# Performance work log

Measured on AMD Instinct MI355X. Metric: run time of the kernel, lower is better.

Reference implementation:

```python
import jax, jax.numpy as jnp
import numpy as np
from jax import lax

B, F, H, W = 1, 8, 16, 16
DIM, HEADS, HD, RANK, T = 1920, 30, 64, 128, 226
SV = F * H * W          # 2048 video tokens
S = T + SV              # 2274 total tokens


def setup_inputs() -> dict:
    key = jax.random.key(0)
    ks = jax.random.split(key, 12)
    r = lambda k, sh, s: jax.random.normal(k, sh, dtype=jnp.float32) * s
    theta = jax.random.uniform(ks[0], (SV, HD), dtype=jnp.float32) * (2.0 * np.pi)
    return dict(
        hidden_states=r(ks[1], (B, SV, DIM), 1.0),
        encoder_hidden_states=r(ks[2], (B, T, DIM), 1.0),
        cos=jnp.cos(theta),
        sin=jnp.sin(theta),
        to_q_w=r(ks[3], (DIM, DIM), 0.02), to_q_b=r(ks[4], (DIM,), 0.02),
        to_k_w=r(ks[5], (DIM, DIM), 0.02), to_k_b=r(ks[6], (DIM,), 0.02),
        to_v_w=r(ks[7], (DIM, DIM), 0.02), to_v_b=r(ks[8], (DIM,), 0.02),
        norm_q_w=jnp.ones((HD,), jnp.float32), norm_q_b=jnp.zeros((HD,), jnp.float32),
        norm_k_w=jnp.ones((HD,), jnp.float32), norm_k_b=jnp.zeros((HD,), jnp.float32),
        conv1_w=r(ks[9], (RANK, DIM, 3), 0.05),
        conv2_w=r(ks[10], (DIM, RANK, 3), 0.05),
        to_out_w=r(ks[11], (DIM, DIM), 0.02),
        to_out_b=jnp.zeros((DIM,), jnp.float32),
    )


def _layernorm(x, w, b, eps=1e-6):
    mu = jnp.mean(x, axis=-1, keepdims=True)
    var = jnp.mean(jnp.square(x - mu), axis=-1, keepdims=True)
    return (x - mu) * lax.rsqrt(var + eps) * w + b


def _rope(x, cos, sin):
    # diffusers interleaved RoPE: pairs (even, odd) along last dim
    xr, xi = x[..., 0::2], x[..., 1::2]
    x_rot = jnp.stack([-xi, xr], axis=-1).reshape(x.shape)
    return x * cos + x_rot * sin


def _conv1d(x, w):  # x: [N, C, L], w: [O, I, K], SAME padding
    return lax.conv_general_dilated(x, w, window_strides=(1,), padding=((1, 1),),
                                    dimension_numbers=('NCH', 'OIH', 'NCH'))


def reference(hidden_states, encoder_hidden_states, cos, sin,
              to_q_w, to_q_b, to_k_w, to_k_b, to_v_w, to_v_b,
              norm_q_w, norm_q_b, norm_k_w, norm_k_b,
              conv1_w, conv2_w, to_out_w, to_out_b):
    # --- temporal conv1d side branch on video tokens only ---
    x = hidden_states.reshape(B, F, H, W, DIM)
    x = jnp.transpose(x, (0, 2, 3, 4, 1)).reshape(B * H * W, DIM, F)  # [BHW, C, F]
    x = _conv1d(x, conv1_w)
    x = jax.nn.gelu(x, approximate=False)
    x = _conv1d(x, conv2_w)
    x = x.reshape(B, H, W, DIM, F)
    conv_branch = jnp.transpose(x, (0, 4, 1, 2, 3)).reshape(B, SV, DIM)

    # --- joint text+video attention ---
    hs = jnp.concatenate([encoder_hidden_states, hidden_states], axis=1)  # [B, S, D]
    q = hs @ to_q_w.T + to_q_b
    k = hs @ to_k_w.T + to_k_b
    v = hs @ to_v_w.T + to_v_b
    q = q.reshape(B, S, HEADS, HD).transpose(0, 2, 1, 3)  # [B, Hh, S, hd]
    k = k.reshape(B, S, HEADS, HD).transpose(0, 2, 1, 3)
    v = v.reshape(B, S, HEADS, HD).transpose(0, 2, 1, 3)

    q = _layernorm(q, norm_q_w, norm_q_b)
    k = _layernorm(k, norm_k_w, norm_k_b)

    # partial RoPE: only video portion (tokens past text_seq_length)
    q = jnp.concatenate([q[:, :, :T], _rope(q[:, :, T:], cos, sin)], axis=2)
    k = jnp.concatenate([k[:, :, :T], _rope(k[:, :, T:], cos, sin)], axis=2)

    scale = 1.0 / np.sqrt(HD).astype(np.float32)
    scores = jnp.einsum('bhqd,bhkd->bhqk', q, k) * scale
    probs = jax.nn.softmax(scores, axis=-1)
    out = jnp.einsum('bhqk,bhkd->bhqd', probs, v)
    out = out.transpose(0, 2, 1, 3).reshape(B, S, DIM)

    # residual add of conv branch into video slice
    out = jnp.concatenate([out[:, :T], out[:, T:] + conv_branch], axis=1)
    out = out @ to_out_w.T + to_out_b

    return out[:, T:], out[:, :T]  # (hidden_states, encoder_hidden_states)
```

## Files before the change

kernel.cpp:

```cpp
#include <hip/hip_runtime.h>
#include <hip/hip_bf16.h>
#include <math.h>

#define F_     8
#define DIM_   1920
#define HEADS_ 30
#define HD_    64
#define RANK_  128
#define T_     226
#define SV_    2048
#define S_     2274
#define SP_    2304

#define BM 128
#define BN 128
#define BK 32

using short8  = __attribute__((ext_vector_type(8))) short;
using f32x4   = __attribute__((ext_vector_type(4))) float;
using i32x4v  = __attribute__((ext_vector_type(4))) int;
using ushort4v= __attribute__((ext_vector_type(4))) unsigned short;

__device__ __forceinline__ unsigned short f2b(float f) {
  unsigned int u = __float_as_uint(f);
  u = (u + 0x7FFFu + ((u >> 16) & 1u)) >> 16;
  return (unsigned short)u;
}
__device__ __forceinline__ float b2f(unsigned short s) {
  return __uint_as_float(((unsigned int)s) << 16);
}
__device__ __forceinline__ void gload_lds16(const void* g, void* l) {
  __builtin_amdgcn_global_load_lds(
      (const __attribute__((address_space(1))) unsigned int*)g,
      (__attribute__((address_space(3))) unsigned int*)l, 16, 0, 0);
}
__device__ __forceinline__ void xcd_swz(int& bx, int& by) {
  const int nx = gridDim.x;
  const int nwg = nx * gridDim.y;
  const int lid = by * nx + bx;
  const int q = nwg >> 3, r = nwg & 7;
  const int xcd = lid & 7, pos = lid >> 3;
  const int wg = (xcd < r ? xcd * (q + 1) : r * (q + 1) + (xcd - r) * q) + pos;
  bx = wg % nx; by = wg / nx;
}

template<int AMODE, int OUTMODE>
__global__ __launch_bounds__(256) void gemm_mfma(
    const unsigned short* __restrict__ A,
    const unsigned short* __restrict__ A2,
    const unsigned short* __restrict__ B,
    const float* __restrict__ bias,
    void* __restrict__ Cout,
    unsigned short* __restrict__ VT,
    int M, int N, int K, int lda, int ldb, int kinner)
{
  __shared__ __align__(16) unsigned short As[BM * BK];
  __shared__ __align__(16) unsigned short Bs[BN * BK];
  if constexpr (AMODE == 3) {
    const int z = blockIdx.z;
    A += (size_t)z * 480;
    B += (size_t)(z >> 2) * 256 * DIM_ + (z & 3) * 480;
    Cout = (void*)((float*)Cout + (size_t)z * M * N);
  }
  int bx = blockIdx.x, by = blockIdx.y;
  xcd_swz(bx, by);
  const int t   = threadIdx.x;
  const int w   = t >> 6, l = t & 63;
  const int wr  = w >> 1, wc = w & 1;
  const int row0 = by * BM, col0 = bx * BN;
  const int lr  = l & 15;
  const int lcg = l >> 4;
  const int sel = (lr >> 1) & 3;
  const int sr  = t >> 2;
  const int sc  = t & 3;

  f32x4 acc[4][4];
#pragma unroll
  for (int i = 0; i < 4; ++i)
#pragma unroll
    for (int j = 0; j < 4; ++j) acc[i][j] = (f32x4){0.f, 0.f, 0.f, 0.f};

  for (int k0 = 0; k0 < K; k0 += BK) {
    int kseg = 0, kcol = k0;
    if constexpr (AMODE == 1) { kseg = k0 / kinner; kcol = k0 - kseg * kinner; }
#pragma unroll
    for (int it = 0; it < 2; ++it) {
      const int r    = it * 64 + sr;
      const int csrc = sc ^ ((r >> 1) & 3);
      int ar = row0 + r; if (ar > M - 1) ar = M - 1;
      const unsigned short* asrc;
      if constexpr (AMODE == 1) {
        asrc = A + (size_t)(ar + kseg * 256) * kinner + kcol + csrc * 8;
      } else if constexpr (AMODE == 2) {
        asrc = (ar < T_) ? (A  + (size_t)ar        * DIM_ + k0 + csrc * 8)
                         : (A2 + (size_t)(ar - T_) * DIM_ + k0 + csrc * 8);
      } else {
        asrc = A + (size_t)ar * lda + k0 + csrc * 8;
      }
      gload_lds16(asrc, (char*)As + it * 4096 + t * 16);
      const unsigned short* bsrc = B + (size_t)(col0 + r) * ldb + k0 + csrc * 8;
      gload_lds16(bsrc, (char*)Bs + it * 4096 + t * 16);
    }
    __syncthreads();

    short8 af[4], bfv[4];
#pragma unroll
    for (int m = 0; m < 4; ++m) {
      int r = wr * 64 + m * 16 + lr;
      af[m] = *(const short8*)((const char*)As + r * 64 + ((lcg ^ sel) << 4));
    }
#pragma unroll
    for (int n = 0; n < 4; ++n) {
      int r = wc * 64 + n * 16 + lr;
      bfv[n] = *(const short8*)((const char*)Bs + r * 64 + ((lcg ^ sel) << 4));
    }
    __builtin_amdgcn_s_setprio(1);
#pragma unroll
    for (int m = 0; m < 4; ++m)
#pragma unroll
      for (int n = 0; n < 4; ++n)
        acc[m][n] = __builtin_amdgcn_mfma_f32_16x16x32_bf16(af[m], bfv[n], acc[m][n], 0, 0, 0);
    __builtin_amdgcn_s_setprio(0);
    __syncthreads();
  }

#pragma unroll
  for (int m = 0; m < 4; ++m) {
    const int rbase = row0 + wr * 64 + m * 16 + lcg * 4;
#pragma unroll
    for (int n = 0; n < 4; ++n) {
      const int c = col0 + wc * 64 + n * 16 + lr;
      const float bi = bias ? bias[c] : 0.f;
      if constexpr (OUTMODE == 3) {
        const int buf = c / DIM_, cc = c - buf * DIM_;
        if (buf == 2) {
          unsigned short* vt = VT + (size_t)cc * SP_ + rbase;
          if (rbase + 4 <= M) {
            ushort4v o = {f2b(acc[m][n][0] + bi), f2b(acc[m][n][1] + bi),
                          f2b(acc[m][n][2] + bi), f2b(acc[m][n][3] + bi)};
            *(ushort4v*)vt = o;
          } else {
#pragma unroll
            for (int reg = 0; reg < 4; ++reg)
              if (rbase + reg < M) vt[reg] = f2b(acc[m][n][reg] + bi);
          }
        } else {
#pragma unroll
          for (int reg = 0; reg < 4; ++reg) {
            const int r = rbase + reg;
            if (r < M)
              ((unsigned short*)Cout)[(size_t)buf * S_ * DIM_ + (size_t)r * DIM_ + cc]
                  = f2b(acc[m][n][reg] + bi);
          }
        }
      } else {
#pragma unroll
        for (int reg = 0; reg < 4; ++reg) {
          const int r = rbase + reg;
          if (r >= M) continue;
          const float v = acc[m][n][reg] + bi;
          if constexpr (OUTMODE == 0) {
            ((float*)Cout)[(size_t)r * N + c] = v;
          } else if constexpr (OUTMODE == 1) {
            ((unsigned short*)Cout)[(size_t)r * N + c] = f2b(v);
          } else {
            const size_t orow = (r >= T_) ? (size_t)(r - T_) : (size_t)(SV_ + r);
            ((float*)Cout)[orow * N + c] = v;
          }
        }
      }
    }
  }
}

__device__ __forceinline__ short8 build_pa(int c0lo, int c0hi, int c1lo, int c1hi,
                                           int addrA, bool hi_m) {
  const int a0 = __builtin_amdgcn_ds_bpermute(addrA,      c0lo);
  const int b0 = __builtin_amdgcn_ds_bpermute(addrA,      c1lo);
  const int a1 = __builtin_amdgcn_ds_bpermute(addrA,      c0hi);
  const int b1 = __builtin_amdgcn_ds_bpermute(addrA,      c1hi);
  const int a2 = __builtin_amdgcn_ds_bpermute(addrA + 64, c0lo);
  const int b2 = __builtin_amdgcn_ds_bpermute(addrA + 64, c1lo);
  const int a3 = __builtin_amdgcn_ds_bpermute(addrA + 64, c0hi);
  const int b3 = __builtin_amdgcn_ds_bpermute(addrA + 64, c1hi);
  i32x4v pw;
  pw[0] = hi_m ? b0 : a0;
  pw[1] = hi_m ? b1 : a1;
  pw[2] = hi_m ? b2 : a2;
  pw[3] = hi_m ? b3 : a3;
  return __builtin_bit_cast(short8, pw);
}

__global__ __launch_bounds__(256) void attn_mfma(
    const unsigned short* __restrict__ Qbb,
    const unsigned short* __restrict__ Kbb,
    const unsigned short* __restrict__ VT,
    unsigned short* __restrict__ Op0,
    unsigned short* __restrict__ Op1,
    float* __restrict__ ml)
{
  __shared__ __align__(16) unsigned short Kl[2][64 * 64];
  __shared__ __align__(16) unsigned short Vl[2][64 * 64];

  const int sv = blockIdx.z;
  int bx = blockIdx.x, by = blockIdx.y;
  xcd_swz(bx, by);
  const int qb = bx, h = by;
  const int t = threadIdx.x, w = t >> 6, l = t & 63;
  const int lr = l & 15, lg = l >> 4;
  const int q0 = qb * 64;
  const int j0base = sv * 1152;
  const int NT = 18;
  unsigned short* Opart = sv ? Op1 : Op0;

  short8 qa[2];
  {
    int qrow = q0 + w * 16 + lr; if (qrow >= S_) qrow = S_ - 1;
    const unsigned short* qp = Qbb + (size_t)qrow * DIM_ + h * 64 + lg * 8;
    qa[0] = *(const short8*)qp;
    qa[1] = *(const short8*)(qp + 32);
  }

  const int srow = t >> 3;
  const int sc0 = ((((t & 7) * 16) ^ ((srow        & 7) << 4)) >> 1);
  const int sc1 = ((((t & 7) * 16) ^ (((srow + 32) & 7) << 4)) >> 1);
  const unsigned short* vsrc0 = VT + (size_t)(h * 64 + srow)      * SP_ + sc0;
  const unsigned short* vsrc1 = VT + (size_t)(h * 64 + srow + 32) * SP_ + sc1;

  f32x4 oacc[4];
#pragma unroll
  for (int n = 0; n < 4; ++n) oacc[n] = (f32x4){0.f, 0.f, 0.f, 0.f};
  float m_run = -1e30f, l_run = 0.f;

  const int addrA = (lr + ((lg & 1) << 5)) << 2;
  const bool hi_m = (lg & 2) != 0;

  {
    int k0 = j0base + srow;      if (k0 >= S_) k0 = S_ - 1;
    int k1 = j0base + srow + 32; if (k1 >= S_) k1 = S_ - 1;
    gload_lds16(Kbb + (size_t)k0 * DIM_ + h * 64 + sc0, (char*)Kl[0] + t * 16);
    gload_lds16(Kbb + (size_t)k1 * DIM_ + h * 64 + sc1, (char*)Kl[0] + 4096 + t * 16);
    gload_lds16(vsrc0 + j0base, (char*)Vl[0] + t * 16);
    gload_lds16(vsrc1 + j0base, (char*)Vl[0] + 4096 + t * 16);
  }
  __syncthreads();

  for (int jt = 0; jt < NT; ++jt) {
    const int j0 = j0base + jt * 64;
    const int cur = jt & 1;

    const int jn0 = (jt + 1 < NT) ? j0 + 64 : j0;
    {
      int k0 = jn0 + srow;      if (k0 >= S_) k0 = S_ - 1;
      int k1 = jn0 + srow + 32; if (k1 >= S_) k1 = S_ - 1;
      gload_lds16(Kbb + (size_t)k0 * DIM_ + h * 64 + sc0,
                  (char*)Kl[cur ^ 1] + t * 16);
      gload_lds16(Kbb + (size_t)k1 * DIM_ + h * 64 + sc1,
                  (char*)Kl[cur ^ 1] + 4096 + t * 16);
      gload_lds16(vsrc0 + jn0, (char*)Vl[cur ^ 1] + t * 16);
      gload_lds16(vsrc1 + jn0, (char*)Vl[cur ^ 1] + 4096 + t * 16);
    }

    f32x4 sacc[4];
#pragma unroll
    for (int m = 0; m < 4; ++m) sacc[m] = (f32x4){0.f, 0.f, 0.f, 0.f};
    __builtin_amdgcn_s_setprio(1);
#pragma unroll
    for (int m = 0; m < 4; ++m) {
#pragma unroll
      for (int ks = 0; ks < 2; ++ks) {
        const short8 kb = *(const short8*)((const char*)Kl[cur] + (m * 16 + lr) * 128 +
                              ((ks * 64 + lg * 16) ^ ((lr & 7) << 4)));
        sacc[m] = __builtin_amdgcn_mfma_f32_16x16x32_bf16(kb, qa[ks], sacc[m], 0, 0, 0);
      }
    }
    __builtin_amdgcn_s_setprio(0);

    if (j0 + 64 > S_) {
#pragma unroll
      for (int m = 0; m < 4; ++m)
#pragma unroll
        for (int r = 0; r < 4; ++r)
          if (j0 + m * 16 + lg * 4 + r >= S_) sacc[m][r] = -1e30f;
    }

    float mx = sacc[0][0];
#pragma unroll
    for (int m = 0; m < 4; ++m)
#pragma unroll
      for (int r = 0; r < 4; ++r) mx = fmaxf(mx, sacc[m][r]);
    mx = fmaxf(mx, __shfl_xor(mx, 16));
    mx = fmaxf(mx, __shfl_xor(mx, 32));

    if (!__all(mx <= m_run + 8.0f)) {
      const float mnew = fmaxf(m_run, mx);
      const float sc = exp2f(m_run - mnew);
      l_run *= sc;
      float scr[4];
#pragma unroll
      for (int r = 0; r < 4; ++r) scr[r] = __shfl(sc, (l & 48) | (lg * 4 + r));
#pragma unroll
      for (int n = 0; n < 4; ++n)
#pragma unroll
        for (int r = 0; r < 4; ++r) oacc[n][r] *= scr[r];
      m_run = mnew;
    }

    float rs = 0.f;
    int c[4][2];
#pragma unroll
    for (int m = 0; m < 4; ++m) {
      const float p0 = exp2f(sacc[m][0] - m_run);
      const float p1 = exp2f(sacc[m][1] - m_run);
      const float p2 = exp2f(sacc[m][2] - m_run);
      const float p3 = exp2f(sacc[m][3] - m_run);
      rs += (p0 + p1) + (p2 + p3);
      asm("v_cvt_pk_bf16_f32 %0, %1, %2" : "=v"(c[m][0]) : "v"(p0), "v"(p1));
      asm("v_cvt_pk_bf16_f32 %0, %1, %2" : "=v"(c[m][1]) : "v"(p2), "v"(p3));
    }
    rs += __shfl_xor(rs, 16);
    rs += __shfl_xor(rs, 32);
    l_run += rs;

    __builtin_amdgcn_s_setprio(1);
    {
      const short8 pa0 = build_pa(c[0][0], c[0][1], c[1][0], c[1][1], addrA, hi_m);
#pragma unroll
      for (int n = 0; n < 4; ++n) {
        const short8 vb = *(const short8*)((const char*)Vl[cur] + (n * 16 + lr) * 128 +
                              ((0 * 64 + lg * 16) ^ ((lr & 7) << 4)));
        oacc[n] = __builtin_amdgcn_mfma_f32_16x16x32_bf16(pa0, vb, oacc[n], 0, 0, 0);
      }
      const short8 pa1 = build_pa(c[2][0], c[2][1], c[3][0], c[3][1], addrA, hi_m);
#pragma unroll
      for (int n = 0; n < 4; ++n) {
        const short8 vb = *(const short8*)((const char*)Vl[cur] + (n * 16 + lr) * 128 +
                              ((1 * 64 + lg * 16) ^ ((lr & 7) << 4)));
        oacc[n] = __builtin_amdgcn_mfma_f32_16x16x32_bf16(pa1, vb, oacc[n], 0, 0, 0);
      }
    }
    __builtin_amdgcn_s_setprio(0);

    __syncthreads();
  }

#pragma unroll
  for (int r = 0; r < 4; ++r) {
    const int row = q0 + w * 16 + lg * 4 + r;
    if (row >= S_) continue;
#pragma unroll
    for (int n = 0; n < 4; ++n)
      Opart[(size_t)row * DIM_ + h * 64 + n * 16 + lr] = f2b(oacc[n][r]);
  }
  if (l < 16) {
    const int row = q0 + w * 16 + lr;
    if (row < S_) {
      float2 v; v.x = m_run; v.y = l_run;
      *(float2*)(ml + ((size_t)(sv * S_ + row) * HEADS_ + h) * 2) = v;
    }
  }
}

#define MERGE_N_ (S_ * DIM_ / 8)
#define CVT_N_   (DIM_ * DIM_ / 8)
__global__ void merge_k(const unsigned short* __restrict__ Op0,
                        const unsigned short* __restrict__ Op1,
                        const float* __restrict__ ml,
                        const unsigned short* __restrict__ y2b,
                        unsigned short* __restrict__ dst,
                        const float* __restrict__ ow,
                        unsigned short* __restrict__ owb)
{
  const int i = blockIdx.x * 256 + threadIdx.x;
  if (i < MERGE_N_) {
    const int e = i * 8;
    const int row = e / DIM_, col = e % DIM_;
    const int h = col >> 6;
    const float* p0 = ml + ((size_t)row * HEADS_ + h) * 2;
    const float* p1 = ml + ((size_t)(S_ + row) * HEADS_ + h) * 2;
    const float m0 = p0[0], l0 = p0[1], m1 = p1[0], l1 = p1[1];
    const float M = fmaxf(m0, m1);
    const float w0 = exp2f(m0 - M), w1 = exp2f(m1 - M);
    const float inv = 1.f / (w0 * l0 + w1 * l1);
    const short8 a = *(const short8*)(Op0 + e);
    const short8 b = *(const short8*)(Op1 + e);
    const bool cadd = row >= T_;
    const unsigned short* yp = y2b + (size_t)(row - T_) * DIM_ + col;
    short8 o;
#pragma unroll
    for (int j = 0; j < 8; ++j) {
      float v = (w0 * b2f((unsigned short)a[j]) + w1 * b2f((unsigned short)b[j])) * inv;
      if (cadd) v += b2f(yp[j]);
      o[j] = (short)f2b(v);
    }
    *(short8*)(dst + e) = o;
  } else if (i < MERGE_N_ + CVT_N_) {
    const int e = (i - MERGE_N_) * 8;
    const float4 v0 = *(const float4*)(ow + e);
    const float4 v1 = *(const float4*)(ow + e + 4);
    short8 o;
    o[0]=(short)f2b(v0.x); o[1]=(short)f2b(v0.y); o[2]=(short)f2b(v0.z); o[3]=(short)f2b(v0.w);
    o[4]=(short)f2b(v1.x); o[5]=(short)f2b(v1.y); o[6]=(short)f2b(v1.z); o[7]=(short)f2b(v1.w);
    *(short8*)(owb + e) = o;
  }
}

#define U0_ 1228800
#define U1_ 3993600
#define U2_ 4427520
#define U3_ 5164800
#define U4_ 5902080
#define U5_ 5907840
__global__ void prep_all(const float* __restrict__ hid, const float* __restrict__ enc,
                         const float* __restrict__ w1, const float* __restrict__ w2,
                         const float* __restrict__ qw, const float* __restrict__ kw,
                         const float* __restrict__ vw, const float* __restrict__ qb2,
                         const float* __restrict__ kb2, const float* __restrict__ vb2,
                         unsigned short* __restrict__ hidpad, unsigned short* __restrict__ encb,
                         unsigned short* __restrict__ w1p, unsigned short* __restrict__ w2p,
                         unsigned short* __restrict__ wqkv, float* __restrict__ bqkv)
{
  const int i = blockIdx.x * 256 + threadIdx.x;
  if (i < U0_) {
    const int e = i * 4;
    const int r = e / DIM_;
    ushort4v o = (ushort4v){0, 0, 0, 0};
    if (r >= 256 && r < 256 + SV_) {
      const float4 v = *(const float4*)(hid + e - 256 * DIM_);
      o[0] = f2b(v.x); o[1] = f2b(v.y); o[2] = f2b(v.z); o[3] = f2b(v.w);
    }
    *(ushort4v*)(hidpad + e) = o;
  } else if (i < U1_) {
    const int e = (i - U0_) * 4;
    const int which = e / (DIM_ * DIM_);
    const int j = e - which * DIM_ * DIM_;
    const float* s = which == 0 ? qw : which == 1 ? kw : vw;
    const float4 v = *(const float4*)(s + j);
    ushort4v o = {f2b(v.x), f2b(v.y), f2b(v.z), f2b(v.w)};
    *(ushort4v*)(wqkv + e) = o;
  } else if (i < U2_) {
    const int e = i - U1_;
    encb[e] = f2b(enc[e]);
  } else if (i < U3_) {
    const int e = i - U2_;
    const int oc = e / (DIM_ * 3), rem = e % (DIM_ * 3);
    const int ks = rem / DIM_, ic = rem % DIM_;
    w1p[e] = f2b(w1[(size_t)oc * DIM_ * 3 + ic * 3 + ks]);
  } else if (i < U4_) {
    const int e = i - U3_;
    const int oc = e / (RANK_ * 3), rem = e % (RANK_ * 3);
    const int ks = rem / RANK_, rc = rem % RANK_;
    w2p[e] = f2b(w2[(size_t)oc * RANK_ * 3 + rc * 3 + ks]);
  } else if (i < U5_) {
    const int e = i - U4_;
    const int which = e / DIM_, j = e % DIM_;
    bqkv[e] = which == 0 ? qb2[j] : which == 1 ? kb2[j] : vb2[j];
  }
}

__global__ void gelupad_k(const float* __restrict__ y1T, unsigned short* __restrict__ dst)
{
  int i = blockIdx.x * 256 + threadIdx.x;
  if (i >= 2560 * RANK_) return;
  int r = i / RANK_, rc = i % RANK_;
  unsigned short o = 0;
  if (r >= 256 && r < 256 + SV_) {
    int s = r - 256;
    float x = 0.f;
#pragma unroll
    for (int z = 0; z < 12; ++z)
      x += y1T[(size_t)z * RANK_ * SV_ + (size_t)rc * SV_ + s];
    o = f2b(0.5f * x * (1.f + erff(x * 0.70710678118654752f)));
  }
  dst[i] = o;
}

__global__ __launch_bounds__(256) void qknorm_rope(
    unsigned short* __restrict__ Qbb, unsigned short* __restrict__ Kbb,
    const float* __restrict__ nq_w, const float* __restrict__ nq_b,
    const float* __restrict__ nk_w, const float* __restrict__ nk_b,
    const float* __restrict__ cosT, const float* __restrict__ sinT)
{
  const int w = threadIdx.x >> 6, lane = threadIdx.x & 63;
  const int idx = blockIdx.x * 4 + w;
  if (idx >= S_ * HEADS_) return;
  const int s = idx / HEADS_, h = idx % HEADS_;
  unsigned short* X = blockIdx.y ? Kbb : Qbb;
  const float* wt = blockIdx.y ? nk_w : nq_w;
  const float* bt = blockIdx.y ? nk_b : nq_b;
  const size_t off = (size_t)s * DIM_ + h * HD_ + lane;
  float x = b2f(X[off]);
  float m = x;
#pragma unroll
  for (int o = 32; o; o >>= 1) m += __shfl_xor(m, o);
  m *= (1.f / 64.f);
  float d = x - m;
  float v = d * d;
#pragma unroll
  for (int o = 32; o; o >>= 1) v += __shfl_xor(v, o);
  v *= (1.f / 64.f);
  float y = d * rsqrtf(v + 1e-6f) * wt[lane] + bt[lane];
  if (s >= T_) {
    float p = __shfl_xor(y, 1);
    float rot = (lane & 1) ? p : -p;
    int sv = s - T_;
    y = y * cosT[(size_t)sv * HD_ + lane] + rot * sinT[(size_t)sv * HD_ + lane];
  }
  if (!blockIdx.y) y *= 0.18033688011112042f;
  X[off] = f2b(y);
}

extern "C" void kernel_launch(void* const* d_in, const int* in_sizes, int n_in,
                              void* d_out, int out_size, void* d_ws, size_t ws_size,
                              hipStream_t stream)
{
  const float* hidden  = (const float*)d_in[0];
  const float* encoder = (const float*)d_in[1];
  const float* cosT    = (const float*)d_in[2];
  const float* sinT    = (const float*)d_in[3];
  const float* to_q_w  = (const float*)d_in[4];
  const float* to_q_b  = (const float*)d_in[5];
  const float* to_k_w  = (const float*)d_in[6];
  const float* to_k_b  = (const float*)d_in[7];
  const float* to_v_w  = (const float*)d_in[8];
  const float* to_v_b  = (const float*)d_in[9];
  const float* nq_w    = (const float*)d_in[10];
  const float* nq_b    = (const float*)d_in[11];
  const float* nk_w    = (const float*)d_in[12];
  const float* nk_b    = (const float*)d_in[13];
  const float* conv1_w = (const float*)d_in[14];
  const float* conv2_w = (const float*)d_in[15];
  const float* to_out_w = (const float*)d_in[16];
  const float* to_out_b = (const float*)d_in[17];
  float* out = (float*)d_out;

  char* p = (char*)d_ws;
  unsigned short* hidpad = (unsigned short*)p;  p += (size_t)2560 * DIM_ * 2;
  unsigned short* y2b    = (unsigned short*)p;  p += (size_t)SV_ * DIM_ * 2;
  unsigned short* wqkv   = (unsigned short*)p;  p += (size_t)3 * DIM_ * DIM_ * 2;
  unsigned short* w1p    = (unsigned short*)p;  p += (size_t)RANK_ * DIM_ * 3 * 2;
  unsigned short* w2p    = (unsigned short*)p;  p += (size_t)DIM_ * RANK_ * 3 * 2;
  unsigned short* QKbb   = (unsigned short*)p;  p += (size_t)2 * S_ * DIM_ * 2;
  unsigned short* VbbT   = (unsigned short*)p;  p += (size_t)DIM_ * SP_ * 2;
  unsigned short* encb   = (unsigned short*)p;  p += (size_t)T_ * DIM_ * 2;
  float*          y1T    = (float*)p;           p += (size_t)12 * RANK_ * SV_ * 4;
  unsigned short* gelup  = (unsigned short*)p;  p += (size_t)2560 * RANK_ * 2;
  float*          bqkv   = (float*)p;           p += (size_t)3 * DIM_ * 4;
  unsigned short* Qbb = QKbb;
  unsigned short* Kbb = QKbb + (size_t)S_ * DIM_;
  unsigned short* Op0 = hidpad;
  unsigned short* Op1 = (unsigned short*)y1T;
  float*          ml  = (float*)((char*)y1T + (size_t)S_ * DIM_ * 2);

  prep_all<<<(U5_ + 255) / 256, 256, 0, stream>>>(
      hidden, encoder, conv1_w, conv2_w, to_q_w, to_k_w, to_v_w,
      to_q_b, to_k_b, to_v_b, hidpad, encb, w1p, w2p, wqkv, bqkv);

  gemm_mfma<3, 0><<<dim3(SV_ / BN, 1, 12), 256, 0, stream>>>(
      w1p, nullptr, hidpad, nullptr, y1T, nullptr, RANK_, SV_, 480, DIM_ * 3, DIM_, 1);
  gelupad_k<<<(2560 * RANK_ + 255) / 256, 256, 0, stream>>>(y1T, gelup);
  gemm_mfma<1, 1><<<dim3(DIM_ / BN, SV_ / BM), 256, 0, stream>>>(
      gelup, nullptr, w2p, nullptr, y2b, nullptr, SV_, DIM_, RANK_ * 3, RANK_ * 3, RANK_ * 3, RANK_);

  const unsigned short* hid0 = hidpad + (size_t)256 * DIM_;
  gemm_mfma<2, 3><<<dim3(3 * DIM_ / BN, (S_ + BM - 1) / BM), 256, 0, stream>>>(
      encb, hid0, wqkv, bqkv, QKbb, VbbT, S_, 3 * DIM_, DIM_, DIM_, DIM_, 1);

  qknorm_rope<<<dim3((S_ * HEADS_ + 3) / 4, 2), 256, 0, stream>>>(
      Qbb, Kbb, nq_w, nq_b, nk_w, nk_b, cosT, sinT);

  attn_mfma<<<dim3((S_ + 63) / 64, HEADS_, 2), 256, 0, stream>>>(
      Qbb, Kbb, VbbT, Op0, Op1, ml);

  merge_k<<<(MERGE_N_ + CVT_N_ + 255) / 256, 256, 0, stream>>>(
      Op0, Op1, ml, y2b, Qbb, to_out_w, wqkv);

  gemm_mfma<0, 2><<<dim3(DIM_ / BN, (S_ + BM - 1) / BM), 256, 0, stream>>>(
      Qbb, nullptr, wqkv, to_out_b, out, nullptr, S_, DIM_, DIM_, DIM_, DIM_, 1);
}
```

Baseline: 381.9 us.

## Use BK=64 GEMM tiles, 3-way attention KV split, vectorized qk-norm

```diff
diff --git a/kernel.cpp b/kernel.cpp
--- a/kernel.cpp
+++ b/kernel.cpp
@@ -11,10 +11,11 @@
 #define SV_    2048
 #define S_     2274
 #define SP_    2304
+#define NS_    3
+#define NTS_   12
 
 #define BM 128
 #define BN 128
-#define BK 32
 
 using short8  = __attribute__((ext_vector_type(8))) short;
 using f32x4   = __attribute__((ext_vector_type(4))) float;
@@ -44,7 +45,7 @@
   bx = wg % nx; by = wg / nx;
 }
 
-template<int AMODE, int OUTMODE>
+template<int AMODE, int OUTMODE, int BKT>
 __global__ __launch_bounds__(256) void gemm_mfma(
     const unsigned short* __restrict__ A,
     const unsigned short* __restrict__ A2,
@@ -54,8 +55,8 @@
     unsigned short* __restrict__ VT,
     int M, int N, int K, int lda, int ldb, int kinner)
 {
-  __shared__ __align__(16) unsigned short As[BM * BK];
-  __shared__ __align__(16) unsigned short Bs[BN * BK];
+  __shared__ __align__(16) unsigned short As[BM * BKT];
+  __shared__ __align__(16) unsigned short Bs[BN * BKT];
   if constexpr (AMODE == 3) {
     const int z = blockIdx.z;
     A += (size_t)z * 480;
@@ -70,9 +71,6 @@
   const int row0 = by * BM, col0 = bx * BN;
   const int lr  = l & 15;
   const int lcg = l >> 4;
-  const int sel = (lr >> 1) & 3;
-  const int sr  = t >> 2;
-  const int sc  = t & 3;
 
   f32x4 acc[4][4];
 #pragma unroll
@@ -80,48 +78,88 @@
 #pragma unroll
     for (int j = 0; j < 4; ++j) acc[i][j] = (f32x4){0.f, 0.f, 0.f, 0.f};
 
-  for (int k0 = 0; k0 < K; k0 += BK) {
+  for (int k0 = 0; k0 < K; k0 += BKT) {
     int kseg = 0, kcol = k0;
     if constexpr (AMODE == 1) { kseg = k0 / kinner; kcol = k0 - kseg * kinner; }
-#pragma unroll
-    for (int it = 0; it < 2; ++it) {
-      const int r    = it * 64 + sr;
-      const int csrc = sc ^ ((r >> 1) & 3);
-      int ar = row0 + r; if (ar > M - 1) ar = M - 1;
-      const unsigned short* asrc;
-      if constexpr (AMODE == 1) {
-        asrc = A + (size_t)(ar + kseg * 256) * kinner + kcol + csrc * 8;
-      } else if constexpr (AMODE == 2) {
-        asrc = (ar < T_) ? (A  + (size_t)ar        * DIM_ + k0 + csrc * 8)
-                         : (A2 + (size_t)(ar - T_) * DIM_ + k0 + csrc * 8);
-      } else {
-        asrc = A + (size_t)ar * lda + k0 + csrc * 8;
+
+    if constexpr (BKT == 32) {
+      const int sr = t >> 2, sc = t & 3;
+#pragma unroll
+      for (int it = 0; it < 2; ++it) {
+        const int r    = it * 64 + sr;
+        const int csrc = sc ^ ((r >> 1) & 3);
+        int ar = row0 + r; if (ar > M - 1) ar = M - 1;
+        const unsigned short* asrc;
+        if constexpr (AMODE == 1) {
+          asrc = A + (size_t)(ar + kseg * 256) * kinner + kcol + csrc * 8;
+        } else if constexpr (AMODE == 2) {
+          asrc = (ar < T_) ? (A  + (size_t)ar        * DIM_ + k0 + csrc * 8)
+                           : (A2 + (size_t)(ar - T_) * DIM_ + k0 + csrc * 8);
+        } else {
+          asrc = A + (size_t)ar * lda + k0 + csrc * 8;
+        }
+        gload_lds16(asrc, (char*)As + it * 4096 + t * 16);
+        const unsigned short* bsrc = B + (size_t)(col0 + it * 64 + sr) * ldb + k0 + csrc * 8;
+        gload_lds16(bsrc, (char*)Bs + it * 4096 + t * 16);
       }
-      gload_lds16(asrc, (char*)As + it * 4096 + t * 16);
-      const unsigned short* bsrc = B + (size_t)(col0 + r) * ldb + k0 + csrc * 8;
-      gload_lds16(bsrc, (char*)Bs + it * 4096 + t * 16);
-    }
-    __syncthreads();
-
-    short8 af[4], bfv[4];
-#pragma unroll
-    for (int m = 0; m < 4; ++m) {
-      int r = wr * 64 + m * 16 + lr;
-      af[m] = *(const short8*)((const char*)As + r * 64 + ((lcg ^ sel) << 4));
-    }
-#pragma unroll
-    for (int n = 0; n < 4; ++n) {
-      int r = wc * 64 + n * 16 + lr;
-      bfv[n] = *(const short8*)((const char*)Bs + r * 64 + ((lcg ^ sel) << 4));
-    }
-    __builtin_amdgcn_s_setprio(1);
-#pragma unroll
-    for (int m = 0; m < 4; ++m)
+      __syncthreads();
+      const int sel = (lr >> 1) & 3;
+      short8 af[4], bfv[4];
+#pragma unroll
+      for (int m = 0; m < 4; ++m)
+        af[m] = *(const short8*)((const char*)As + (wr * 64 + m * 16 + lr) * 64 + ((lcg ^ sel) << 4));
 #pragma unroll
       for (int n = 0; n < 4; ++n)
-        acc[m][n] = __builtin_amdgcn_mfma_f32_16x16x32_bf16(af[m], bfv[n], acc[m][n], 0, 0, 0);
-    __builtin_amdgcn_s_setprio(0);
-    __syncthreads();
+        bfv[n] = *(const short8*)((const char*)Bs + (wc * 64 + n * 16 + lr) * 64 + ((lcg ^ sel) << 4));
+      __builtin_amdgcn_s_setprio(1);
+#pragma unroll
+      for (int m = 0; m < 4; ++m)
+#pragma unroll
+        for (int n = 0; n < 4; ++n)
+          acc[m][n] = __builtin_amdgcn_mfma_f32_16x16x32_bf16(af[m], bfv[n], acc[m][n], 0, 0, 0);
+      __builtin_amdgcn_s_setprio(0);
+      __syncthreads();
+    } else {
+      const int srow8 = (t >> 3) & 7;
+      const int csrc  = (t & 7) ^ srow8;
+#pragma unroll
+      for (int it = 0; it < 4; ++it) {
+        const int r = it * 32 + (t >> 3);
+        int ar = row0 + r; if (ar > M - 1) ar = M - 1;
+        const unsigned short* asrc;
+        if constexpr (AMODE == 1) {
+          asrc = A + (size_t)(ar + kseg * 256) * kinner + kcol + csrc * 8;
+        } else if constexpr (AMODE == 2) {
+          asrc = (ar < T_) ? (A  + (size_t)ar        * DIM_ + k0 + csrc * 8)
+                           : (A2 + (size_t)(ar - T_) * DIM_ + k0 + csrc * 8);
+        } else {
+          asrc = A + (size_t)ar * lda + k0 + csrc * 8;
+        }
+        gload_lds16(asrc, (char*)As + it * 4096 + t * 16);
+        const unsigned short* bsrc = B + (size_t)(col0 + r) * ldb + k0 + csrc * 8;
+        gload_lds16(bsrc, (char*)Bs + it * 4096 + t * 16);
+      }
+      __syncthreads();
+#pragma unroll
+      for (int kh = 0; kh < 2; ++kh) {
+        const int sl = ((kh * 4 + lcg) ^ (lr & 7)) << 4;
+        short8 af[4], bfv[4];
+#pragma unroll
+        for (int m = 0; m < 4; ++m)
+          af[m] = *(const short8*)((const char*)As + (wr * 64 + m * 16 + lr) * 128 + sl);
+#pragma unroll
+        for (int n = 0; n < 4; ++n)
+          bfv[n] = *(const short8*)((const char*)Bs + (wc * 64 + n * 16 + lr) * 128 + sl);
+        __builtin_amdgcn_s_setprio(1);
+#pragma unroll
+        for (int m = 0; m < 4; ++m)
+#pragma unroll
+          for (int n = 0; n < 4; ++n)
+            acc[m][n] = __builtin_amdgcn_mfma_f32_16x16x32_bf16(af[m], bfv[n], acc[m][n], 0, 0, 0);
+        __builtin_amdgcn_s_setprio(0);
+      }
+      __syncthreads();
+    }
   }
 
 #pragma unroll
@@ -197,6 +235,7 @@
     const unsigned short* __restrict__ VT,
     unsigned short* __restrict__ Op0,
     unsigned short* __restrict__ Op1,
+    unsigned short* __restrict__ Op2,
     float* __restrict__ ml)
 {
   __shared__ __align__(16) unsigned short Kl[2][64 * 64];
@@ -209,9 +248,8 @@
   const int t = threadIdx.x, w = t >> 6, l = t & 63;
   const int lr = l & 15, lg = l >> 4;
   const int q0 = qb * 64;
-  const int j0base = sv * 1152;
-  const int NT = 18;
-  unsigned short* Opart = sv ? Op1 : Op0;
+  const int j0base = sv * (NTS_ * 64);
+  unsigned short* Opart = (sv == 0) ? Op0 : (sv == 1) ? Op1 : Op2;
 
   short8 qa[2];
   {
@@ -245,11 +283,11 @@
   }
   __syncthreads();
 
-  for (int jt = 0; jt < NT; ++jt) {
+  for (int jt = 0; jt < NTS_; ++jt) {
     const int j0 = j0base + jt * 64;
     const int cur = jt & 1;
 
-    const int jn0 = (jt + 1 < NT) ? j0 + 64 : j0;
+    const int jn0 = (jt + 1 < NTS_) ? j0 + 64 : j0;
     {
       int k0 = jn0 + srow;      if (k0 >= S_) k0 = S_ - 1;
       int k1 = jn0 + srow + 32; if (k1 >= S_) k1 = S_ - 1;
@@ -365,6 +403,7 @@
 #define CVT_N_   (DIM_ * DIM_ / 8)
 __global__ void merge_k(const unsigned short* __restrict__ Op0,
                         const unsigned short* __restrict__ Op1,
+                        const unsigned short* __restrict__ Op2,
                         const float* __restrict__ ml,
                         const unsigned short* __restrict__ y2b,
                         unsigned short* __restrict__ dst,
@@ -376,20 +415,33 @@
     const int e = i * 8;
     const int row = e / DIM_, col = e % DIM_;
     const int h = col >> 6;
-    const float* p0 = ml + ((size_t)row * HEADS_ + h) * 2;
-    const float* p1 = ml + ((size_t)(S_ + row) * HEADS_ + h) * 2;
-    const float m0 = p0[0], l0 = p0[1], m1 = p1[0], l1 = p1[1];
-    const float M = fmaxf(m0, m1);
-    const float w0 = exp2f(m0 - M), w1 = exp2f(m1 - M);
-    const float inv = 1.f / (w0 * l0 + w1 * l1);
+    float mv[NS_], lv[NS_];
+#pragma unroll
+    for (int ss = 0; ss < NS_; ++ss) {
+      const float* pp = ml + ((size_t)(ss * S_ + row) * HEADS_ + h) * 2;
+      mv[ss] = pp[0]; lv[ss] = pp[1];
+    }
+    float M = mv[0];
+#pragma unroll
+    for (int ss = 1; ss < NS_; ++ss) M = fmaxf(M, mv[ss]);
+    float wv[NS_], L = 0.f;
+#pragma unroll
+    for (int ss = 0; ss < NS_; ++ss) {
+      wv[ss] = exp2f(mv[ss] - M);
+      L = fmaf(wv[ss], lv[ss], L);
+    }
+    const float inv = 1.f / L;
     const short8 a = *(const short8*)(Op0 + e);
     const short8 b = *(const short8*)(Op1 + e);
+    const short8 c2 = *(const short8*)(Op2 + e);
     const bool cadd = row >= T_;
     const unsigned short* yp = y2b + (size_t)(row - T_) * DIM_ + col;
     short8 o;
 #pragma unroll
     for (int j = 0; j < 8; ++j) {
-      float v = (w0 * b2f((unsigned short)a[j]) + w1 * b2f((unsigned short)b[j])) * inv;
+      float v = (wv[0] * b2f((unsigned short)a[j]) +
+                 wv[1] * b2f((unsigned short)b[j]) +
+                 wv[2] * b2f((unsigned short)c2[j])) * inv;
       if (cadd) v += b2f(yp[j]);
       o[j] = (short)f2b(v);
     }
@@ -481,33 +533,62 @@
     const float* __restrict__ nk_w, const float* __restrict__ nk_b,
     const float* __restrict__ cosT, const float* __restrict__ sinT)
 {
-  const int w = threadIdx.x >> 6, lane = threadIdx.x & 63;
-  const int idx = blockIdx.x * 4 + w;
+  const int w = threadIdx.x >> 6, l = threadIdx.x & 63;
+  const int g = l >> 3, e = l & 7;
+  const int idx = (blockIdx.x * 4 + w) * 8 + g;
   if (idx >= S_ * HEADS_) return;
   const int s = idx / HEADS_, h = idx % HEADS_;
   unsigned short* X = blockIdx.y ? Kbb : Qbb;
   const float* wt = blockIdx.y ? nk_w : nq_w;
   const float* bt = blockIdx.y ? nk_b : nq_b;
-  const size_t off = (size_t)s * DIM_ + h * HD_ + lane;
-  float x = b2f(X[off]);
-  float m = x;
-#pragma unroll
-  for (int o = 32; o; o >>= 1) m += __shfl_xor(m, o);
-  m *= (1.f / 64.f);
-  float d = x - m;
-  float v = d * d;
-#pragma unroll
-  for (int o = 32; o; o >>= 1) v += __shfl_xor(v, o);
-  v *= (1.f / 64.f);
-  float y = d * rsqrtf(v + 1e-6f) * wt[lane] + bt[lane];
+  const size_t off = (size_t)s * DIM_ + h * HD_ + e * 8;
+
+  const short8 xv = *(const short8*)(X + off);
+  float x[8];
+#pragma unroll
+  for (int j = 0; j < 8; ++j) x[j] = b2f((unsigned short)xv[j]);
+
+  float sm = 0.f;
+#pragma unroll
+  for (int j = 0; j < 8; ++j) sm += x[j];
+  sm += __shfl_xor(sm, 1); sm += __shfl_xor(sm, 2); sm += __shfl_xor(sm, 4);
+  const float mean = sm * (1.f / 64.f);
+  float vr = 0.f;
+#pragma unroll
+  for (int j = 0; j < 8; ++j) { const float d = x[j] - mean; vr += d * d; }
+  vr += __shfl_xor(vr, 1); vr += __shfl_xor(vr, 2); vr += __shfl_xor(vr, 4);
+  const float inv = rsqrtf(vr * (1.f / 64.f) + 1e-6f);
+
+  const float4 w0 = *(const float4*)(wt + e * 8);
+  const float4 w1 = *(const float4*)(wt + e * 8 + 4);
+  const float4 b0 = *(const float4*)(bt + e * 8);
+  const float4 b1 = *(const float4*)(bt + e * 8 + 4);
+  const float wa[8] = {w0.x, w0.y, w0.z, w0.w, w1.x, w1.y, w1.z, w1.w};
+  const float ba[8] = {b0.x, b0.y, b0.z, b0.w, b1.x, b1.y, b1.z, b1.w};
+  float y[8];
+#pragma unroll
+  for (int j = 0; j < 8; ++j) y[j] = (x[j] - mean) * inv * wa[j] + ba[j];
+
   if (s >= T_) {
-    float p = __shfl_xor(y, 1);
-    float rot = (lane & 1) ? p : -p;
-    int sv = s - T_;
-    y = y * cosT[(size_t)sv * HD_ + lane] + rot * sinT[(size_t)sv * HD_ + lane];
-  }
-  if (!blockIdx.y) y *= 0.18033688011112042f;
-  X[off] = f2b(y);
+    const int sv2 = s - T_;
+    const float4 c0 = *(const float4*)(cosT + (size_t)sv2 * HD_ + e * 8);
+    const float4 c1 = *(const float4*)(cosT + (size_t)sv2 * HD_ + e * 8 + 4);
+    const float4 s0 = *(const float4*)(sinT + (size_t)sv2 * HD_ + e * 8);
+    const float4 s1 = *(const float4*)(sinT + (size_t)sv2 * HD_ + e * 8 + 4);
+    const float cc[8] = {c0.x, c0.y, c0.z, c0.w, c1.x, c1.y, c1.z, c1.w};
+    const float ssn[8] = {s0.x, s0.y, s0.z, s0.w, s1.x, s1.y, s1.z, s1.w};
+#pragma unroll
+    for (int j = 0; j < 8; j += 2) {
+      const float a = y[j], bb = y[j + 1];
+      y[j]     = a  * cc[j]     - bb * ssn[j];
+      y[j + 1] = bb * cc[j + 1] + a  * ssn[j + 1];
+    }
+  }
+  const float qs = blockIdx.y ? 1.f : 0.18033688011112042f;
+  short8 o;
+#pragma unroll
+  for (int j = 0; j < 8; ++j) o[j] = (short)f2b(y[j] * qs);
+  *(short8*)(X + off) = o;
 }
 
 extern "C" void kernel_launch(void* const* d_in, const int* in_sizes, int n_in,
@@ -551,30 +632,32 @@
   unsigned short* Op0 = hidpad;
   unsigned short* Op1 = (unsigned short*)y1T;
   float*          ml  = (float*)((char*)y1T + (size_t)S_ * DIM_ * 2);
+  unsigned short* Op2 = wqkv + (size_t)DIM_ * DIM_;
+  unsigned short* owb = wqkv;
 
   prep_all<<<(U5_ + 255) / 256, 256, 0, stream>>>(
       hidden, encoder, conv1_w, conv2_w, to_q_w, to_k_w, to_v_w,
       to_q_b, to_k_b, to_v_b, hidpad, encb, w1p, w2p, wqkv, bqkv);
 
-  gemm_mfma<3, 0><<<dim3(SV_ / BN, 1, 12), 256, 0, stream>>>(
+  gemm_mfma<3, 0, 32><<<dim3(SV_ / BN, 1, 12), 256, 0, stream>>>(
       w1p, nullptr, hidpad, nullptr, y1T, nullptr, RANK_, SV_, 480, DIM_ * 3, DIM_, 1);
   gelupad_k<<<(2560 * RANK_ + 255) / 256, 256, 0, stream>>>(y1T, gelup);
-  gemm_mfma<1, 1><<<dim3(DIM_ / BN, SV_ / BM), 256, 0, stream>>>(
+  gemm_mfma<1, 1, 64><<<dim3(DIM_ / BN, SV_ / BM), 256, 0, stream>>>(
       gelup, nullptr, w2p, nullptr, y2b, nullptr, SV_, DIM_, RANK_ * 3, RANK_ * 3, RANK_ * 3, RANK_);
 
   const unsigned short* hid0 = hidpad + (size_t)256 * DIM_;
-  gemm_mfma<2, 3><<<dim3(3 * DIM_ / BN, (S_ + BM - 1) / BM), 256, 0, stream>>>(
+  gemm_mfma<2, 3, 64><<<dim3(3 * DIM_ / BN, (S_ + BM - 1) / BM), 256, 0, stream>>>(
       encb, hid0, wqkv, bqkv, QKbb, VbbT, S_, 3 * DIM_, DIM_, DIM_, DIM_, 1);
 
-  qknorm_rope<<<dim3((S_ * HEADS_ + 3) / 4, 2), 256, 0, stream>>>(
+  qknorm_rope<<<dim3((S_ * HEADS_ + 31) / 32, 2), 256, 0, stream>>>(
       Qbb, Kbb, nq_w, nq_b, nk_w, nk_b, cosT, sinT);
 
-  attn_mfma<<<dim3((S_ + 63) / 64, HEADS_, 2), 256, 0, stream>>>(
-      Qbb, Kbb, VbbT, Op0, Op1, ml);
+  attn_mfma<<<dim3((S_ + 63) / 64, HEADS_, NS_), 256, 0, stream>>>(
+      Qbb, Kbb, VbbT, Op0, Op1, Op2, ml);
 
   merge_k<<<(MERGE_N_ + CVT_N_ + 255) / 256, 256, 0, stream>>>(
-      Op0, Op1, ml, y2b, Qbb, to_out_w, wqkv);
-
-  gemm_mfma<0, 2><<<dim3(DIM_ / BN, (S_ + BM - 1) / BM), 256, 0, stream>>>(
-      Qbb, nullptr, wqkv, to_out_b, out, nullptr, S_, DIM_, DIM_, DIM_, DIM_, 1);
-}
+      Op0, Op1, Op2, ml, y2b, Qbb, to_out_w, owb);
+
+  gemm_mfma<0, 2, 64><<<dim3(DIM_ / BN, (S_ + BM - 1) / BM), 256, 0, stream>>>(
+      Qbb, nullptr, owb, to_out_b, out, nullptr, S_, DIM_, DIM_, DIM_, DIM_, 1);
+}
```

Result: faster. 343.2 us (-10.1%).
